# Kernel optimization log

Measured on AMD Instinct MI355X. Metric: run time of the kernel, lower is better.

The kernel has to match this reference:

```python
import jax, jax.numpy as jnp
import numpy as np

Q, N, D = 4096, 100000, 128


def setup_inputs() -> dict:
    key = jax.random.key(0)
    k1, k2, k3 = jax.random.split(key, 3)
    inputs = jax.random.normal(k1, (Q, D), dtype=jnp.float32)
    X_train = jax.random.normal(k2, (N, D), dtype=jnp.float32)
    y_train = jax.random.normal(k3, (N,), dtype=jnp.float32)
    return {"inputs": inputs, "X_train": X_train, "y_train": y_train, "k": 32}


def reference(inputs, X_train, y_train, k):
    # Squared Euclidean distances [Q, N] via the expanded identity
    # |a-b|^2 = |a|^2 + |b|^2 - 2 a.b  (avoids materializing [Q, N, D]).
    q_sq = jnp.sum(inputs * inputs, axis=-1, keepdims=True)        # [Q, 1]
    t_sq = jnp.sum(X_train * X_train, axis=-1)                     # [N]
    cross = jnp.einsum('qd,nd->qn', inputs, X_train)               # [Q, N]
    distances = q_sq + t_sq[None, :] - 2.0 * cross                 # [Q, N]
    # top_k of -distances == k nearest neighbors
    _, indices = jax.lax.top_k(-distances, k)                      # [Q, k]
    nearest = y_train[indices]                                     # [Q, k]
    return jnp.mean(nearest, axis=1)                               # [Q]
```

## Files before the change

kernel.cpp:

```cpp
#include <hip/hip_runtime.h>
#include <hip/hip_fp16.h>
#include <cstdint>
#include <cstddef>


constexpr int Q_  = 4096;
constexpr int N_  = 100000;
constexpr int D_  = 128;
constexpr int K_  = 32;

constexpr int QT    = 32;
constexpr int BN    = 256;
constexpr int NCH   = 8;
constexpr int CHUNK = 12544;
constexpr int ITERS = CHUNK / BN;
constexpr int NPAD  = NCH * CHUNK;
constexpr int CW    = 128;
constexpr int QTS   = 16;
constexpr int SAMP_M      = 8192;
constexpr int SAMP_STRIDE = 12;
constexpr int SAMP_OFF    = 5;
constexpr int SAMP_ITERS  = SAMP_M / BN;

constexpr int XS_B  = NPAD / 64;
constexpr int SAM_B = SAMP_M / 64;
constexpr int PQ_B  = Q_ / 4;
constexpr int MXN   = XS_B * 4;

typedef __attribute__((ext_vector_type(8))) _Float16 half8;
typedef __attribute__((ext_vector_type(4))) float    floatx4;
typedef unsigned long long ull;

#define DEV __device__ __forceinline__
constexpr ull DEADC = ~0ull;

DEV ull pack_cand(float score, unsigned int n) {
    unsigned int s = __float_as_uint(score);
    s = (s & 0x80000000u) ? ~s : (s | 0x80000000u);
    return ((ull)s << 32) | (ull)n;
}
DEV float unpack_score(ull k) {
    unsigned int s = (unsigned int)(k >> 32);
    s = (s & 0x80000000u) ? (s ^ 0x80000000u) : ~s;
    return __uint_as_float(s);
}
DEV ull u64min(ull a, ull b) { return a < b ? a : b; }
DEV float inf_f() { return __int_as_float(0x7f800000); }

DEV ull bitonic64(ull v, int L) {
    #pragma unroll
    for (int k2 = 2; k2 <= 64; k2 <<= 1)
        #pragma unroll
        for (int j2 = k2 >> 1; j2 >= 1; j2 >>= 1) {
            ull o = __shfl_xor(v, j2);
            bool up = ((L & k2) == 0);
            bool lo = ((L & j2) == 0);
            ull mn = u64min(v, o), mx = v ^ o ^ mn;
            v = (lo == up) ? mn : mx;
        }
    return v;
}
DEV ull bimerge64(ull v, int L) {
    #pragma unroll
    for (int j2 = 32; j2 >= 1; j2 >>= 1) {
        ull o = __shfl_xor(v, j2);
        ull mn = u64min(v, o), mx = v ^ o ^ mn;
        v = ((L & j2) == 0) ? mn : mx;
    }
    return v;
}

__global__ void prep_all(const float* __restrict__ X, const float* __restrict__ Qm,
                         __half* __restrict__ Xs, float* __restrict__ tsq,
                         float* __restrict__ mxArr, float* __restrict__ mxArrH,
                         __half* __restrict__ Xsam, float* __restrict__ tsqS,
                         __half* __restrict__ Qh,
                         float* __restrict__ qsq, float* __restrict__ qrs,
                         int* __restrict__ flagF)
{
    const int tid = threadIdx.x, L = tid & 63, wv = tid >> 6;
    const int bx = blockIdx.x;
    const int am = L & 15, aq = L >> 4;

    if (bx < XS_B) {
        int t16 = bx * 4 + wv;
        int r = t16 * 16 + am;
        float ssq = 0.f, xr2 = 0.f, xh2 = 0.f;
        #pragma unroll
        for (int ks = 0; ks < 4; ++ks) {
            int c = ks * 32 + aq * 8;
            float v0=0,v1=0,v2=0,v3=0,v4=0,v5=0,v6=0,v7=0;
            if (r < N_) {
                float4 a = *(const float4*)(X + (size_t)r * D_ + c);
                float4 b = *(const float4*)(X + (size_t)r * D_ + c + 4);
                v0=a.x; v1=a.y; v2=a.z; v3=a.w; v4=b.x; v5=b.y; v6=b.z; v7=b.w;
            }
            half8 h;
            h[0]=(_Float16)v0; h[1]=(_Float16)v1; h[2]=(_Float16)v2; h[3]=(_Float16)v3;
            h[4]=(_Float16)v4; h[5]=(_Float16)v5; h[6]=(_Float16)v6; h[7]=(_Float16)v7;
            float c0=(float)h[0], c1=(float)h[1], c2=(float)h[2], c3=(float)h[3];
            float c4=(float)h[4], c5=(float)h[5], c6=(float)h[6], c7=(float)h[7];
            float r0=v0-c0, r1=v1-c1, r2=v2-c2, r3=v3-c3;
            float r4=v4-c4, r5=v5-c5, r6=v6-c6, r7=v7-c7;
            ssq += v0*v0+v1*v1+v2*v2+v3*v3+v4*v4+v5*v5+v6*v6+v7*v7;
            xr2 += r0*r0+r1*r1+r2*r2+r3*r3+r4*r4+r5*r5+r6*r6+r7*r7;
            xh2 += c0*c0+c1*c1+c2*c2+c3*c3+c4*c4+c5*c5+c6*c6+c7*c7;
            *(half8*)(Xs + ((size_t)(t16 * 4 + ks)) * 512 + L * 8) = h;
        }
        ssq += __shfl_xor(ssq, 16); ssq += __shfl_xor(ssq, 32);
        xr2 += __shfl_xor(xr2, 16); xr2 += __shfl_xor(xr2, 32);
        xh2 += __shfl_xor(xh2, 16); xh2 += __shfl_xor(xh2, 32);
        if (aq == 0) tsq[r] = (r < N_) ? ssq : inf_f();
        float m = xr2;
        m = fmaxf(m, __shfl_xor(m, 1)); m = fmaxf(m, __shfl_xor(m, 2));
        m = fmaxf(m, __shfl_xor(m, 4)); m = fmaxf(m, __shfl_xor(m, 8));
        float mh = xh2;
        mh = fmaxf(mh, __shfl_xor(mh, 1)); mh = fmaxf(mh, __shfl_xor(mh, 2));
        mh = fmaxf(mh, __shfl_xor(mh, 4)); mh = fmaxf(mh, __shfl_xor(mh, 8));
        if (L == 0) { mxArr[t16] = m; mxArrH[t16] = mh; }
    } else if (bx < XS_B + SAM_B) {
        int t16 = (bx - XS_B) * 4 + wv;
        int j = t16 * 16 + am;
        int n = j * SAMP_STRIDE + SAMP_OFF;
        float ssq = 0.f;
        #pragma unroll
        for (int ks = 0; ks < 4; ++ks) {
            int c = ks * 32 + aq * 8;
            float4 a = *(const float4*)(X + (size_t)n * D_ + c);
            float4 b = *(const float4*)(X + (size_t)n * D_ + c + 4);
            half8 h;
            h[0]=(_Float16)a.x; h[1]=(_Float16)a.y; h[2]=(_Float16)a.z; h[3]=(_Float16)a.w;
            h[4]=(_Float16)b.x; h[5]=(_Float16)b.y; h[6]=(_Float16)b.z; h[7]=(_Float16)b.w;
            ssq += a.x*a.x + a.y*a.y + a.z*a.z + a.w*a.w
                 + b.x*b.x + b.y*b.y + b.z*b.z + b.w*b.w;
            *(half8*)(Xsam + ((size_t)(t16 * 4 + ks)) * 512 + L * 8) = h;
        }
        ssq += __shfl_xor(ssq, 16); ssq += __shfl_xor(ssq, 32);
        if (aq == 0) tsqS[j] = ssq;
    } else {
        int r = (bx - XS_B - SAM_B) * 4 + wv;
        float2 x = *(const float2*)(Qm + (size_t)r * D_ + 2 * L);
        __half h0 = __float2half(x.x), h1 = __float2half(x.y);
        size_t o = (size_t)r * D_ + 2 * L;
        Qh[o] = h0; Qh[o + 1] = h1;
        float r0 = x.x - __half2float(h0), r1 = x.y - __half2float(h1);
        float s  = x.x * x.x + x.y * x.y;
        float sr = r0 * r0 + r1 * r1;
        s  += __shfl_xor(s, 32);  s += __shfl_xor(s, 16);  s += __shfl_xor(s, 8);
        s  += __shfl_xor(s, 4);   s += __shfl_xor(s, 2);   s += __shfl_xor(s, 1);
        sr += __shfl_xor(sr, 32); sr += __shfl_xor(sr, 16); sr += __shfl_xor(sr, 8);
        sr += __shfl_xor(sr, 4);  sr += __shfl_xor(sr, 2);  sr += __shfl_xor(sr, 1);
        if (L == 0) { qsq[r] = s; qrs[r] = sr; flagF[r] = 0; }
    }
}

__global__ void reduce_mx(const float* __restrict__ mxArr,
                          const float* __restrict__ mxArrH,
                          float* __restrict__ mxOut)
{
    __shared__ float sR[4], sH[4];
    const int tid = threadIdx.x, L = tid & 63, wv = tid >> 6;
    float a = 0.f, b = 0.f;
    #pragma unroll 1
    for (int i = tid; i < MXN; i += 256) {
        a = fmaxf(a, mxArr[i]);
        b = fmaxf(b, mxArrH[i]);
    }
    #pragma unroll
    for (int s = 32; s; s >>= 1) {
        a = fmaxf(a, __shfl_xor(a, s));
        b = fmaxf(b, __shfl_xor(b, s));
    }
    if (L == 0) { sR[wv] = a; sH[wv] = b; }
    __syncthreads();
    if (tid == 0) {
        mxOut[0] = fmaxf(fmaxf(sR[0], sR[1]), fmaxf(sR[2], sR[3]));
        mxOut[1] = fmaxf(fmaxf(sH[0], sH[1]), fmaxf(sH[2], sH[3]));
    }
}

__global__ __launch_bounds__(256, 2) void sample_T(
    const __half* __restrict__ Qh, const __half* __restrict__ Xsam,
    const float* __restrict__ tsqS, const float* __restrict__ qsq,
    const float* __restrict__ qrs, const float* __restrict__ mxOut,
    float* __restrict__ Teff, float* __restrict__ rawT, float* __restrict__ EwA)
{
    __shared__ float sT[QTS][130];
    const int tid = threadIdx.x, L = tid & 63, wv = tid >> 6;
    const int qbase = blockIdx.x * QTS;
    const int nwv = wv * 64;
    const int am = L & 15, aq = L >> 4;

    half8 afh[4];
    #pragma unroll
    for (int ks = 0; ks < 4; ++ks) {
        size_t o = (size_t)(qbase + am) * D_ + ks * 32 + aq * 8;
        afh[ks] = *(const half8*)(Qh + o);
    }

    float t2a[4], t2b[4];
    #pragma unroll
    for (int rg = 0; rg < 4; ++rg) { t2a[rg] = inf_f(); t2b[rg] = inf_f(); }

    const __half* bp = Xsam + (size_t)nwv * 128 + (size_t)L * 8;
    const float*  tp = tsqS + nwv + am;

    half8 bc[4], bn[4];
    #pragma unroll
    for (int nt = 0; nt < 4; ++nt)
        bc[nt] = *(const half8*)(bp + nt * 2048);

    #pragma unroll 1
    for (int it = 0; it < SAMP_ITERS; ++it) {
        float ts[4];
        #pragma unroll
        for (int nt = 0; nt < 4; ++nt) ts[nt] = tp[nt * 16];

        floatx4 acc[4] = {};
        #pragma unroll
        for (int ks = 0; ks < 4; ++ks) {
            const __half* pp = (ks < 3) ? (bp + (ks + 1) * 512) : (bp + 32768);
            #pragma unroll
            for (int nt = 0; nt < 4; ++nt)
                bn[nt] = *(const half8*)(pp + nt * 2048);
            #pragma unroll
            for (int nt = 0; nt < 4; ++nt)
                acc[nt] = __builtin_amdgcn_mfma_f32_16x16x32_f16(
                    afh[ks], bc[nt], acc[nt], 0, 0, 0);
            #pragma unroll
            for (int nt = 0; nt < 4; ++nt) bc[nt] = bn[nt];
        }
        #pragma unroll
        for (int rg = 0; rg < 4; ++rg) {
            float m1 = t2a[rg], m2 = t2b[rg];
            #pragma unroll
            for (int nt = 0; nt < 4; ++nt) {
                float v = ts[nt] - 2.f * acc[nt][rg];
                if (v < m2) { if (v < m1) { m2 = m1; m1 = v; } else m2 = v; }
            }
            t2a[rg] = m1; t2b[rg] = m2;
        }
        bp += 32768; tp += BN;
    }
    #pragma unroll
    for (int rg = 0; rg < 4; ++rg) {
        int q = aq * 4 + rg;
        sT[q][wv * 32 + am * 2 + 0] = t2a[rg];
        sT[q][wv * 32 + am * 2 + 1] = t2b[rg];
    }
    __syncthreads();

    const float mxr = mxOut[0], mxh = mxOut[1];

    #pragma unroll 1
    for (int j = 0; j < 4; ++j) {
        int q = wv * 4 + j;
        float a = sT[q][2 * L], b = sT[q][2 * L + 1];
        float g = 0.f;
        #pragma unroll 1
        for (int r = 0; r < 16; ++r) {
            float mn = fminf(a, b);
            mn = fminf(mn, __shfl_xor(mn, 32)); mn = fminf(mn, __shfl_xor(mn, 16));
            mn = fminf(mn, __shfl_xor(mn, 8));  mn = fminf(mn, __shfl_xor(mn, 4));
            mn = fminf(mn, __shfl_xor(mn, 2));  mn = fminf(mn, __shfl_xor(mn, 1));
            g = mn;
            ull ba = __ballot(a == g);
            if (ba) { if (L == __ffsll(ba) - 1) a = inf_f(); }
            else    { ull bb = __ballot(b == g); if (L == __ffsll(bb) - 1) b = inf_f(); }
        }
        if (L == 0) {
            int gq = qbase + q;
            float e = 2.f * (sqrtf(qsq[gq]) * sqrtf(mxr)
                           + sqrtf(qrs[gq]) * sqrtf(mxh)) + 0.02f;
            rawT[gq] = g; EwA[gq] = e; Teff[gq] = g + e;
        }
    }
}

__global__ __launch_bounds__(256, 2) void knn_main(
    const __half* __restrict__ Qh, const __half* __restrict__ Xs,
    const float* __restrict__ tsq, const float* __restrict__ Teff,
    ull* __restrict__ candG, int* __restrict__ cntC, int* __restrict__ flagF)
{
    __shared__ ull candL[QT][CW];
    __shared__ int cntL[QT];

    const int tid = threadIdx.x, L = tid & 63, wv = tid >> 6;
    const int lb = blockIdx.x, ch = lb & 7;
    const int qbase = (lb >> 3) * QT, chBase = ch * CHUNK, nwv = wv * 64;
    const int am = L & 15, aq = L >> 4;

    if (tid < QT) cntL[tid] = 0;
    __syncthreads();

    float th[2][4];
    float nH[2];
    #pragma unroll
    for (int qt = 0; qt < 2; ++qt) {
        #pragma unroll
        for (int rg = 0; rg < 4; ++rg)
            th[qt][rg] = Teff[qbase + qt * 16 + aq * 4 + rg];
        float m = fmaxf(fmaxf(th[qt][0], th[qt][1]), fmaxf(th[qt][2], th[qt][3]));
        nH[qt] = -0.5f * m - 1e-3f;
    }

    half8 afh[2][4];
    #pragma unroll
    for (int qt = 0; qt < 2; ++qt)
        #pragma unroll
        for (int ks = 0; ks < 4; ++ks) {
            size_t o = (size_t)(qbase + qt * 16 + am) * D_ + ks * 32 + aq * 8;
            afh[qt][ks] = *(const half8*)(Qh + o);
        }

    const __half* bp = Xs + (size_t)(chBase + nwv) * 128 + (size_t)L * 8;
    const float*  tp = tsq + chBase + nwv + am;
    int n0 = chBase + nwv + am;

    half8 bx[8], by[8];
    #pragma unroll
    for (int j = 0; j < 8; ++j)
        bx[j] = *(const half8*)(bp + (j >> 2) * 512 + (j & 3) * 2048);

    #pragma unroll 1
    for (int it = 0; it < ITERS; ++it) {
        float ts[4];
        #pragma unroll
        for (int nt = 0; nt < 4; ++nt) ts[nt] = tp[nt * 16];

        floatx4 acc[2][4] = {};

        #pragma unroll
        for (int j = 0; j < 8; ++j)
            by[j] = *(const half8*)(bp + (2 + (j >> 2)) * 512 + (j & 3) * 2048);
        #pragma unroll
        for (int ks = 0; ks < 2; ++ks)
            #pragma unroll
            for (int nt = 0; nt < 4; ++nt) {
                acc[0][nt] = __builtin_amdgcn_mfma_f32_16x16x32_f16(
                    afh[0][ks], bx[ks * 4 + nt], acc[0][nt], 0, 0, 0);
                acc[1][nt] = __builtin_amdgcn_mfma_f32_16x16x32_f16(
                    afh[1][ks], bx[ks * 4 + nt], acc[1][nt], 0, 0, 0);
            }

        #pragma unroll
        for (int j = 0; j < 8; ++j)
            bx[j] = *(const half8*)(bp + 32768 + (j >> 2) * 512 + (j & 3) * 2048);
        #pragma unroll
        for (int ks = 0; ks < 2; ++ks)
            #pragma unroll
            for (int nt = 0; nt < 4; ++nt) {
                acc[0][nt] = __builtin_amdgcn_mfma_f32_16x16x32_f16(
                    afh[0][2 + ks], by[ks * 4 + nt], acc[0][nt], 0, 0, 0);
                acc[1][nt] = __builtin_amdgcn_mfma_f32_16x16x32_f16(
                    afh[1][2 + ks], by[ks * 4 + nt], acc[1][nt], 0, 0, 0);
            }

        unsigned hit = 0;
        #pragma unroll
        for (int nt = 0; nt < 4; ++nt) {
            #pragma unroll
            for (int qt = 0; qt < 2; ++qt) {
                float mx = fmaxf(fmaxf(acc[qt][nt][0], acc[qt][nt][1]),
                                 fmaxf(acc[qt][nt][2], acc[qt][nt][3]));
                float Gm = fmaf(0.5f, ts[nt], nH[qt]);
                if (mx > Gm) hit |= 1u << (nt * 2 + qt);
            }
        }
        if (__any(hit != 0)) {
            #pragma unroll
            for (int nt = 0; nt < 4; ++nt) {
                #pragma unroll
                for (int qt = 0; qt < 2; ++qt) {
                    if (!__any(hit & (1u << (nt * 2 + qt)))) continue;
                    unsigned n = (unsigned)(n0 + nt * 16);
                    #pragma unroll
                    for (int rg = 0; rg < 4; ++rg) {
                        float s = fmaf(-2.f, acc[qt][nt][rg], ts[nt]);
                        if (s < th[qt][rg]) {
                            int q = qt * 16 + aq * 4 + rg;
                            int pos = atomicAdd(&cntL[q], 1);
                            if (pos < CW)
                                candL[q][pos] = pack_cand(s, n);
                            else
                                flagF[qbase + q] = 1;
                        }
                    }
                }
            }
        }
        bp += 32768; tp += BN; n0 += BN;
    }

    __syncthreads();

    #pragma unroll 1
    for (int j = 0; j < 8; ++j) {
        int q = wv * 8 + j;
        int gq = qbase + q;
        int c = cntL[q];
        int cc = c < CW ? c : CW;
        ull* dst = candG + ((size_t)gq * NCH + ch) * CW;
        #pragma unroll
        for (int off = 0; off < CW; off += 64)
            if (off + L < cc) dst[off + L] = candL[q][off + L];
        if (L == 0) cntC[gq * NCH + ch] = cc;
    }
}

__global__ void finalize(const ull* __restrict__ candG, const int* __restrict__ cntC,
                         const int* __restrict__ flagF, const float* __restrict__ Qm,
                         const float* __restrict__ X, const float* __restrict__ tsq,
                         const float* __restrict__ rawT, const float* __restrict__ EwA,
                         const float* __restrict__ Ytr, float* __restrict__ out)
{
    __shared__ ull fb[4][256];
    int L = threadIdx.x & 63;
    int wv = threadIdx.x >> 6;
    int q = blockIdx.x * 4 + wv;
    bool bad = (flagF[q] != 0);
    float result = 0.f;

    if (!bad) {
        int cg = (L < NCH) ? cntC[q * NCH + L] : 0;
        int ctot = cg;
        ctot += __shfl_xor(ctot, 32); ctot += __shfl_xor(ctot, 16);
        ctot += __shfl_xor(ctot, 8);  ctot += __shfl_xor(ctot, 4);
        ctot += __shfl_xor(ctot, 2);  ctot += __shfl_xor(ctot, 1);
        if (ctot < K_) bad = true;
        else {
            ull s = DEADC;
            #pragma unroll 1
            for (int g = 0; g < NCH; ++g) {
                int c_g = __shfl(cg, g);
                const ull* cb = candG + ((size_t)q * NCH + g) * CW;
                #pragma unroll 1
                for (int off = 0; off < c_g; off += 64) {
                    ull v = (off + L < c_g) ? cb[off + L] : DEADC;
                    v = bitonic64(v, L);
                    ull w = __shfl(v, 63 - L);
                    s = bimerge64(u64min(s, w), L);
                }
            }
            int cr = ctot < 64 ? ctot : 64;
            unsigned n = (unsigned)(s & 0xffffffffu);
            ull pe = DEADC;
            if (L < cr) {
                const float4* xp = (const float4*)(X + (size_t)n * D_);
                const float4* qp = (const float4*)(Qm + (size_t)q * D_);
                float d = 0.f;
                #pragma unroll 8
                for (int i = 0; i < 32; ++i) {
                    float4 xv = xp[i], qv = qp[i];
                    d += qv.x * xv.x + qv.y * xv.y + qv.z * xv.z + qv.w * xv.w;
                }
                pe = pack_cand(tsq[n] - 2.f * d, n);
            }
            ull pe2 = bitonic64(pe, L);
            float exact31 = unpack_score(__shfl(pe2, K_ - 1));
            bool ok = exact31 < rawT[q];
            if (ctot > 64) {
                float A63 = unpack_score(__shfl(s, 63));
                ok = ok && (A63 - EwA[q] > exact31);
            }
            if (!ok) bad = true;
            else {
                float ys = 0.f;
                if (L < K_) ys = Ytr[(unsigned)(pe2 & 0xffffffffu)];
                ys += __shfl_xor(ys, 32); ys += __shfl_xor(ys, 16);
                ys += __shfl_xor(ys, 8);  ys += __shfl_xor(ys, 4);
                ys += __shfl_xor(ys, 2);  ys += __shfl_xor(ys, 1);
                result = ys * (1.f / K_);
            }
        }
    }

    if (bad) {
        const float4* qp = (const float4*)(Qm + (size_t)q * D_);
        float T = rawT[q] + EwA[q];
        float lo = 0.f, hi = 0.f;
        bool haveLo = false, haveHi = false;
        int cnt = 0;
        #pragma unroll 1
        for (int att = 0; att < 40; ++att) {
            cnt = 0;
            #pragma unroll 1
            for (int j = 0; j < NPAD / 64; ++j) {
                int n = j * 64 + L;
                float s = inf_f();
                if (n < N_) {
                    const float4* xp = (const float4*)(X + (size_t)n * D_);
                    float d = 0.f;
                    #pragma unroll 4
                    for (int i = 0; i < 32; ++i) {
                        float4 xv = xp[i], qv = qp[i];
                        d += qv.x * xv.x + qv.y * xv.y + qv.z * xv.z + qv.w * xv.w;
                    }
                    s = tsq[n] - 2.f * d;
                }
                bool want = s < T;
                ull m = __ballot(want);
                if (m) {
                    int pos = cnt + (int)__popcll(m & ((1ull << L) - 1ull));
                    if (want && pos < 256) fb[wv][pos] = pack_cand(s, (unsigned)n);
                    cnt += (int)__popcll(m);
                }
            }
            if (cnt >= K_ && cnt <= 256) break;
            if (cnt < K_) { lo = T; haveLo = true;
                T = haveHi ? 0.5f * (T + hi) : T + exp2f((float)att) * 0.5f; }
            else { hi = T; haveHi = true;
                T = haveLo ? 0.5f * (lo + T) : T - exp2f((float)att) * 0.5f; }
        }
        if (cnt >= K_ && cnt <= 256) {
            ull s64 = DEADC;
            #pragma unroll 1
            for (int off = 0; off < 256; off += 64) {
                if (off >= cnt) break;
                ull v = (off + L < cnt) ? fb[wv][off + L] : DEADC;
                v = bitonic64(v, L);
                ull w = __shfl(v, 63 - L);
                s64 = bimerge64(u64min(s64, w), L);
            }
            float ys = (L < K_) ? Ytr[(unsigned)(s64 & 0xffffffffu)] : 0.f;
            ys += __shfl_xor(ys, 32); ys += __shfl_xor(ys, 16);
            ys += __shfl_xor(ys, 8);  ys += __shfl_xor(ys, 4);
            ys += __shfl_xor(ys, 2);  ys += __shfl_xor(ys, 1);
            result = ys * (1.f / K_);
        } else {
            ull last = 0;
            float ysum = 0.f;
            for (int r = 0; r < K_; ++r) {
                ull best = DEADC;
                for (int j = 0; j < NPAD / 64; ++j) {
                    int n = j * 64 + L;
                    if (n < N_) {
                        const float4* xp = (const float4*)(X + (size_t)n * D_);
                        float d = 0.f;
                        #pragma unroll 4
                        for (int i = 0; i < 32; ++i) {
                            float4 xv = xp[i], qv = qp[i];
                            d += qv.x * xv.x + qv.y * xv.y + qv.z * xv.z + qv.w * xv.w;
                        }
                        ull k = pack_cand(tsq[n] - 2.f * d, n);
                        if (k > last && k < best) best = k;
                    }
                }
                best = u64min(best, __shfl_xor(best, 32));
                best = u64min(best, __shfl_xor(best, 16));
                best = u64min(best, __shfl_xor(best, 8));
                best = u64min(best, __shfl_xor(best, 4));
                best = u64min(best, __shfl_xor(best, 2));
                best = u64min(best, __shfl_xor(best, 1));
                if (L == 0) ysum += Ytr[(unsigned)(best & 0xffffffffu)];
                last = best;
            }
            result = ysum * (1.f / K_);
        }
    }
    if (L == 0) out[q] = result;
}

extern "C" void kernel_launch(void* const* d_in, const int* in_sizes, int n_in,
                              void* d_out, int out_size, void* d_ws, size_t ws_size,
                              hipStream_t stream)
{
    const float* Qm  = (const float*)d_in[0];
    const float* X   = (const float*)d_in[1];
    const float* Ytr = (const float*)d_in[2];
    float* out = (float*)d_out;

    char* w = (char*)d_ws;
    auto alloc = [&](size_t bytes) {
        char* p = w; w += (bytes + 255) & ~(size_t)255; return p;
    };
    __half* Xs   = (__half*)  alloc((size_t)(NPAD + BN) * D_ * 2);
    __half* Qh   = (__half*)  alloc((size_t)Q_ * D_ * 2);
    float*  ts   = (float*)   alloc((size_t)NPAD * 4);
    __half* Xsm  = (__half*)  alloc((size_t)(SAMP_M + BN) * D_ * 2);
    float*  tsS  = (float*)   alloc((size_t)SAMP_M * 4);
    ull*    cd   = (ull*)     alloc((size_t)Q_ * NCH * CW * 8);
    int*    cnC  = (int*)     alloc((size_t)Q_ * NCH * 4);
    int*    flg  = (int*)     alloc((size_t)Q_ * 4);
    float*  mxA  = (float*)   alloc((size_t)MXN * 4);
    float*  mxAH = (float*)   alloc((size_t)MXN * 4);
    float*  mxO  = (float*)   alloc(256);
    float*  Tef  = (float*)   alloc((size_t)Q_ * 4);
    float*  rwT  = (float*)   alloc((size_t)Q_ * 4);
    float*  Ew   = (float*)   alloc((size_t)Q_ * 4);
    float*  qs   = (float*)   alloc((size_t)Q_ * 4);
    float*  qr2  = (float*)   alloc((size_t)Q_ * 4);

    prep_all<<<XS_B + SAM_B + PQ_B, 256, 0, stream>>>(
        X, Qm, Xs, ts, mxA, mxAH, Xsm, tsS, Qh, qs, qr2, flg);
    reduce_mx<<<1, 256, 0, stream>>>(mxA, mxAH, mxO);
    sample_T<<<Q_ / QTS, 256, 0, stream>>>(Qh, Xsm, tsS, qs, qr2, mxO,
                                           Tef, rwT, Ew);
    knn_main<<<(Q_ / QT) * NCH, 256, 0, stream>>>(Qh, Xs, ts, Tef, cd, cnC, flg);
    finalize<<<Q_ / 4, 256, 0, stream>>>(cd, cnC, flg, Qm, X, ts, rwT, Ew, Ytr, out);
}
```

Before: 405.6 us.

## Split each N-chunk into two halves to double knn_main grid

Each 12544-row chunk is split into two sub-chunks (6400 and 6144 rows), which doubles the number of knn_main blocks from 1024 to 2048 and halves the per-block loop length. Per-block candidate capacity drops from 128 to 64, and finalize now merges 16 sub-lists of up to 64 candidates each, skipping empty ones. The aim is better occupancy and load balance across CUs, plus a simpler merge with one bitonic pass per sub-list. The cost is that Q fragments and thresholds are loaded twice as often, and the smaller capacity makes fallback on overflow more likely.

```diff
diff --git a/kernel.cpp b/kernel.cpp
--- a/kernel.cpp
+++ b/kernel.cpp
@@ -12,10 +12,11 @@
 constexpr int QT    = 32;
 constexpr int BN    = 256;
 constexpr int NCH   = 8;
+constexpr int NSUB  = 16;
 constexpr int CHUNK = 12544;
-constexpr int ITERS = CHUNK / BN;
+constexpr int HALF0 = 6400;
 constexpr int NPAD  = NCH * CHUNK;
-constexpr int CW    = 128;
+constexpr int CWS   = 64;
 constexpr int QTS   = 16;
 constexpr int SAMP_M      = 8192;
 constexpr int SAMP_STRIDE = 12;
@@ -282,12 +283,15 @@
     const float* __restrict__ tsq, const float* __restrict__ Teff,
     ull* __restrict__ candG, int* __restrict__ cntC, int* __restrict__ flagF)
 {
-    __shared__ ull candL[QT][CW];
+    __shared__ ull candL[QT][CWS];
     __shared__ int cntL[QT];
 
     const int tid = threadIdx.x, L = tid & 63, wv = tid >> 6;
     const int lb = blockIdx.x, ch = lb & 7;
-    const int qbase = (lb >> 3) * QT, chBase = ch * CHUNK, nwv = wv * 64;
+    const int half = (lb >> 3) & 1, sub = lb & 15;
+    const int qbase = (lb >> 4) * QT, nwv = wv * 64;
+    const int rowBase = ch * CHUNK + half * HALF0;
+    const int iters = half ? 24 : 25;
     const int am = L & 15, aq = L >> 4;
 
     if (tid < QT) cntL[tid] = 0;
@@ -313,9 +317,9 @@
             afh[qt][ks] = *(const half8*)(Qh + o);
         }
 
-    const __half* bp = Xs + (size_t)(chBase + nwv) * 128 + (size_t)L * 8;
-    const float*  tp = tsq + chBase + nwv + am;
-    int n0 = chBase + nwv + am;
+    const __half* bp = Xs + (size_t)(rowBase + nwv) * 128 + (size_t)L * 8;
+    const float*  tp = tsq + rowBase + nwv + am;
+    int n0 = rowBase + nwv + am;
 
     half8 bx[8], by[8];
     #pragma unroll
@@ -323,7 +327,7 @@
         bx[j] = *(const half8*)(bp + (j >> 2) * 512 + (j & 3) * 2048);
 
     #pragma unroll 1
-    for (int it = 0; it < ITERS; ++it) {
+    for (int it = 0; it < iters; ++it) {
         float ts[4];
         #pragma unroll
         for (int nt = 0; nt < 4; ++nt) ts[nt] = tp[nt * 16];
@@ -380,7 +384,7 @@
                         if (s < th[qt][rg]) {
                             int q = qt * 16 + aq * 4 + rg;
                             int pos = atomicAdd(&cntL[q], 1);
-                            if (pos < CW)
+                            if (pos < CWS)
                                 candL[q][pos] = pack_cand(s, n);
                             else
                                 flagF[qbase + q] = 1;
@@ -399,12 +403,10 @@
         int q = wv * 8 + j;
         int gq = qbase + q;
         int c = cntL[q];
-        int cc = c < CW ? c : CW;
-        ull* dst = candG + ((size_t)gq * NCH + ch) * CW;
-        #pragma unroll
-        for (int off = 0; off < CW; off += 64)
-            if (off + L < cc) dst[off + L] = candL[q][off + L];
-        if (L == 0) cntC[gq * NCH + ch] = cc;
+        int cc = c < CWS ? c : CWS;
+        ull* dst = candG + ((size_t)gq * NSUB + sub) * CWS;
+        if (L < cc) dst[L] = candL[q][L];
+        if (L == 0) cntC[gq * NSUB + sub] = cc;
     }
 }
 
@@ -422,7 +424,7 @@
     float result = 0.f;
 
     if (!bad) {
-        int cg = (L < NCH) ? cntC[q * NCH + L] : 0;
+        int cg = (L < NSUB) ? cntC[q * NSUB + L] : 0;
         int ctot = cg;
         ctot += __shfl_xor(ctot, 32); ctot += __shfl_xor(ctot, 16);
         ctot += __shfl_xor(ctot, 8);  ctot += __shfl_xor(ctot, 4);
@@ -431,16 +433,14 @@
         else {
             ull s = DEADC;
             #pragma unroll 1
-            for (int g = 0; g < NCH; ++g) {
+            for (int g = 0; g < NSUB; ++g) {
                 int c_g = __shfl(cg, g);
-                const ull* cb = candG + ((size_t)q * NCH + g) * CW;
-                #pragma unroll 1
-                for (int off = 0; off < c_g; off += 64) {
-                    ull v = (off + L < c_g) ? cb[off + L] : DEADC;
-                    v = bitonic64(v, L);
-                    ull w = __shfl(v, 63 - L);
-                    s = bimerge64(u64min(s, w), L);
-                }
+                if (c_g == 0) continue;
+                const ull* cb = candG + ((size_t)q * NSUB + g) * CWS;
+                ull v = (L < c_g) ? cb[L] : DEADC;
+                v = bitonic64(v, L);
+                ull w = __shfl(v, 63 - L);
+                s = bimerge64(u64min(s, w), L);
             }
             int cr = ctot < 64 ? ctot : 64;
             unsigned n = (unsigned)(s & 0xffffffffu);
@@ -579,8 +579,8 @@
     float*  ts   = (float*)   alloc((size_t)NPAD * 4);
     __half* Xsm  = (__half*)  alloc((size_t)(SAMP_M + BN) * D_ * 2);
     float*  tsS  = (float*)   alloc((size_t)SAMP_M * 4);
-    ull*    cd   = (ull*)     alloc((size_t)Q_ * NCH * CW * 8);
-    int*    cnC  = (int*)     alloc((size_t)Q_ * NCH * 4);
+    ull*    cd   = (ull*)     alloc((size_t)Q_ * NSUB * CWS * 8);
+    int*    cnC  = (int*)     alloc((size_t)Q_ * NSUB * 4);
     int*    flg  = (int*)     alloc((size_t)Q_ * 4);
     float*  mxA  = (float*)   alloc((size_t)MXN * 4);
     float*  mxAH = (float*)   alloc((size_t)MXN * 4);
@@ -596,6 +596,6 @@
     reduce_mx<<<1, 256, 0, stream>>>(mxA, mxAH, mxO);
     sample_T<<<Q_ / QTS, 256, 0, stream>>>(Qh, Xsm, tsS, qs, qr2, mxO,
                                            Tef, rwT, Ew);
-    knn_main<<<(Q_ / QT) * NCH, 256, 0, stream>>>(Qh, Xs, ts, Tef, cd, cnC, flg);
+    knn_main<<<(Q_ / QT) * NSUB, 256, 0, stream>>>(Qh, Xs, ts, Tef, cd, cnC, flg);
     finalize<<<Q_ / 4, 256, 0, stream>>>(cd, cnC, flg, Qm, X, ts, rwT, Ew, Ytr, out);
 }
```

Result: no change. 400.6 us (median of 2 runs) (-1.2%).
